# Kernel optimization log

Measured on AMD Instinct MI355X. Metric: run time of the kernel, lower is better.

## Reference

```python
import jax, jax.numpy as jnp
import numpy as np

N_HEADS = 12


def setup_inputs() -> dict:
    key = jax.random.key(0)
    ks = jax.random.split(key, 4)
    B, T, C = 1, 4096, 768
    x = jax.random.normal(ks[0], (B, T, C), dtype=jnp.float32)
    w_qkv = jax.random.normal(ks[1], (C, 3 * C), dtype=jnp.float32) * (C ** -0.5)
    b_qkv = jnp.zeros((3 * C,), dtype=jnp.float32)
    w_proj = jax.random.normal(ks[2], (C, C), dtype=jnp.float32) * (C ** -0.5)
    b_proj = jnp.zeros((C,), dtype=jnp.float32)
    return {"x": x, "w_qkv": w_qkv, "b_qkv": b_qkv, "w_proj": w_proj, "b_proj": b_proj}


def reference(x, w_qkv, b_qkv, w_proj, b_proj):
    B, T, C = x.shape
    H = N_HEADS
    hd = C // H
    qkv = x @ w_qkv + b_qkv                      # [B,T,3C]
    q, k, v = jnp.split(qkv, 3, axis=-1)
    # [B,H,T,hd]
    q = q.reshape(B, T, H, hd).transpose(0, 2, 1, 3)
    k = k.reshape(B, T, H, hd).transpose(0, 2, 1, 3)
    v = v.reshape(B, T, H, hd).transpose(0, 2, 1, 3)
    scale = 1.0 / jnp.sqrt(jnp.float32(hd))
    attn = jnp.einsum('bhqd,bhkd->bhqk', q, k) * scale  # [B,H,T,T]
    causal = jnp.tril(jnp.ones((T, T), dtype=bool))
    attn = jnp.where(causal, attn, jnp.float32(-jnp.inf))
    attn = jax.nn.softmax(attn, axis=-1)
    out = jnp.einsum('bhqk,bhkd->bhqd', attn, v)        # [B,H,T,hd]
    out = out.transpose(0, 2, 1, 3).reshape(B, T, C)
    return out @ w_proj + b_proj
```

## Files before the change

### kernel.cpp

```cpp
#include <hip/hip_runtime.h>
#include <hip/hip_bf16.h>


#define T_SEQ 4096
#define C_DIM 768
#define C3    2304
#define NH    12
#define HD    64

typedef __attribute__((ext_vector_type(8))) short bf16x8;
typedef __attribute__((ext_vector_type(4))) short bf16x4;
typedef __attribute__((ext_vector_type(4))) float f32x4;

__device__ inline unsigned short f2bf(float f) {
  union { float f; unsigned u; } v; v.f = f;
  unsigned r = v.u + 0x7fff + ((v.u >> 16) & 1);
  return (unsigned short)(r >> 16);
}
__device__ inline unsigned short f2bf_trunc(float f) {
  union { float f; unsigned u; } v; v.f = f;
  return (unsigned short)(v.u >> 16);
}

__device__ inline void gl2lds16(const void* g, void* l) {
  __builtin_amdgcn_global_load_lds(
      (const __attribute__((address_space(1))) unsigned int*)g,
      (__attribute__((address_space(3))) unsigned int*)l, 16, 0, 0);
}

#if __has_builtin(__builtin_amdgcn_exp2f)
#define EXP2F(x) __builtin_amdgcn_exp2f(x)
#else
#define EXP2F(x) exp2f(x)
#endif

#define NB_CONV  (T_SEQ * C_DIM / 2048)
#define NB_TQKV  ((C3 / 32) * (C_DIM / 32))
#define NB_TPROJ ((C_DIM / 32) * (C_DIM / 32))

__global__ __launch_bounds__(256) void prep_fused(
    const float* __restrict__ x, const float* __restrict__ w_qkv,
    const float* __restrict__ w_proj, unsigned short* __restrict__ xb,
    unsigned short* __restrict__ wqkvT, unsigned short* __restrict__ wprojT) {
  __shared__ float t[32][33];
  const int b = blockIdx.x;
  const int tid = threadIdx.x;

  if (b < NB_CONV) {
    int i = (b * 256 + tid) * 8;
    float4 v0 = *(const float4*)(x + i);
    float4 v1 = *(const float4*)(x + i + 4);
    unsigned short o[8] = {f2bf(v0.x), f2bf(v0.y), f2bf(v0.z), f2bf(v0.w),
                           f2bf(v1.x), f2bf(v1.y), f2bf(v1.z), f2bf(v1.w)};
    *(uint4*)(xb + i) = *(uint4*)o;
    return;
  }
  const float* in;
  unsigned short* outT;
  int R, Cc, bi;
  if (b < NB_CONV + NB_TQKV) {
    in = w_qkv; outT = wqkvT; R = C_DIM; Cc = C3; bi = b - NB_CONV;
  } else {
    in = w_proj; outT = wprojT; R = C_DIM; Cc = C_DIM; bi = b - NB_CONV - NB_TQKV;
  }
  const int tx = tid & 31, ty = tid >> 5;
  const int c0 = (bi % (Cc / 32)) * 32, r0 = (bi / (Cc / 32)) * 32;
#pragma unroll
  for (int i = 0; i < 4; ++i) {
    int r = ty + i * 8;
    t[r][tx] = in[(size_t)(r0 + r) * Cc + c0 + tx];
  }
  __syncthreads();
#pragma unroll
  for (int i = 0; i < 4; ++i) {
    int c = ty + i * 8;
    outT[(size_t)(c0 + c) * R + r0 + tx] = f2bf(t[tx][c]);
  }
}

__global__ __launch_bounds__(256) void gemm_qkv(
    const unsigned short* __restrict__ A, const unsigned short* __restrict__ Bt,
    const float* __restrict__ bias, unsigned short* __restrict__ Cq,
    unsigned short* __restrict__ vTp, int M, int N, int K) {
  __shared__ unsigned short As[128 * 64];
  __shared__ unsigned short Bs[128 * 64];
  const int tid = threadIdx.x;
  const int wave = tid >> 6, lane = tid & 63;
  const int lo = lane & 15, g8 = lane >> 4;
  const int lo7 = lo & 7;
  const int wm = wave >> 1, wn = wave & 1;
  const int bm = blockIdx.y * 128, bn = blockIdx.x * 128;
  const int drow8 = lane >> 3;
  const int dslot = (lane & 7) * 8;
  const int dsrc = ((lane & 7) ^ drow8) * 8;

  f32x4 acc[4][4];
#pragma unroll
  for (int mt = 0; mt < 4; ++mt)
#pragma unroll
    for (int nt = 0; nt < 4; ++nt) acc[mt][nt] = (f32x4){0.f, 0.f, 0.f, 0.f};

  const unsigned short* Abase = A + (size_t)bm * K;
  const unsigned short* Bbase = Bt + (size_t)bn * K;

  for (int k0 = 0; k0 < K; k0 += 64) {
    __syncthreads();
#pragma unroll
    for (int p = 0; p < 4; ++p) {
      const int r = p * 32 + wave * 8 + drow8;
      gl2lds16(Abase + (size_t)r * K + k0 + dsrc, As + r * 64 + dslot);
      gl2lds16(Bbase + (size_t)r * K + k0 + dsrc, Bs + r * 64 + dslot);
    }
    __syncthreads();

#pragma unroll
    for (int kk = 0; kk < 2; ++kk) {
      bf16x8 a[4], b[4];
#pragma unroll
      for (int mt = 0; mt < 4; ++mt)
        a[mt] = *(const bf16x8*)(
            As + (wm * 64 + mt * 16 + lo) * 64 + (((kk * 4 + g8) ^ lo7) * 8));
#pragma unroll
      for (int nt = 0; nt < 4; ++nt)
        b[nt] = *(const bf16x8*)(
            Bs + (wn * 64 + nt * 16 + lo) * 64 + (((kk * 4 + g8) ^ lo7) * 8));
#pragma unroll
      for (int mt = 0; mt < 4; ++mt)
#pragma unroll
        for (int nt = 0; nt < 4; ++nt)
          acc[mt][nt] = __builtin_amdgcn_mfma_f32_16x16x32_bf16(a[mt], b[nt], acc[mt][nt], 0, 0, 0);
    }
  }

  if (bn < 2 * C_DIM) {
    const float sc = (bn < C_DIM) ? 0.18033688011112042f : 1.0f;
#pragma unroll
    for (int nt = 0; nt < 4; ++nt) {
      const int n = bn + wn * 64 + nt * 16 + lo;
      const float bv = bias[n];
#pragma unroll
      for (int mt = 0; mt < 4; ++mt)
#pragma unroll
        for (int r = 0; r < 4; ++r) {
          const int m = bm + wm * 64 + mt * 16 + g8 * 4 + r;
          Cq[(size_t)m * C3 + n] = f2bf((acc[mt][nt][r] + bv) * sc);
        }
    }
  } else {
#pragma unroll
    for (int nt = 0; nt < 4; ++nt) {
      const int n = bn + wn * 64 + nt * 16 + lo;
      const float bv = bias[n];
      unsigned short* row = vTp + (size_t)(n - 2 * C_DIM) * T_SEQ;
#pragma unroll
      for (int mt = 0; mt < 4; ++mt) {
        const int mbase = (bm + wm * 64 + mt * 16 + g8 * 4) & ~31;
        bf16x4 o4;
#pragma unroll
        for (int r = 0; r < 4; ++r) o4[r] = (short)f2bf(acc[mt][nt][r] + bv);
        *(bf16x4*)(row + mbase + 8 * g8 + 4 * (mt & 1)) = o4;
      }
    }
  }
}

__global__ __launch_bounds__(256) void gemm_bt_mfma(
    const unsigned short* __restrict__ A, const unsigned short* __restrict__ Bt,
    const float* __restrict__ bias, float* __restrict__ C,
    int M, int N, int K) {
  __shared__ unsigned short As[128 * 64];
  __shared__ unsigned short Bs[128 * 64];
  const int tid = threadIdx.x;
  const int wave = tid >> 6, lane = tid & 63;
  const int lo = lane & 15, g8 = lane >> 4;
  const int lo7 = lo & 7;
  const int wm = wave >> 1, wn = wave & 1;
  const int bm = blockIdx.y * 128, bn = blockIdx.x * 128;
  const int drow8 = lane >> 3;
  const int dslot = (lane & 7) * 8;
  const int dsrc = ((lane & 7) ^ drow8) * 8;

  f32x4 acc[4][4];
#pragma unroll
  for (int mt = 0; mt < 4; ++mt)
#pragma unroll
    for (int nt = 0; nt < 4; ++nt) acc[mt][nt] = (f32x4){0.f, 0.f, 0.f, 0.f};

  const unsigned short* Abase = A + (size_t)bm * K;
  const unsigned short* Bbase = Bt + (size_t)bn * K;

  for (int k0 = 0; k0 < K; k0 += 64) {
    __syncthreads();
#pragma unroll
    for (int p = 0; p < 4; ++p) {
      const int r = p * 32 + wave * 8 + drow8;
      gl2lds16(Abase + (size_t)r * K + k0 + dsrc, As + r * 64 + dslot);
      gl2lds16(Bbase + (size_t)r * K + k0 + dsrc, Bs + r * 64 + dslot);
    }
    __syncthreads();

#pragma unroll
    for (int kk = 0; kk < 2; ++kk) {
      bf16x8 a[4], b[4];
#pragma unroll
      for (int mt = 0; mt < 4; ++mt)
        a[mt] = *(const bf16x8*)(
            As + (wm * 64 + mt * 16 + lo) * 64 + (((kk * 4 + g8) ^ lo7) * 8));
#pragma unroll
      for (int nt = 0; nt < 4; ++nt)
        b[nt] = *(const bf16x8*)(
            Bs + (wn * 64 + nt * 16 + lo) * 64 + (((kk * 4 + g8) ^ lo7) * 8));
#pragma unroll
      for (int mt = 0; mt < 4; ++mt)
#pragma unroll
        for (int nt = 0; nt < 4; ++nt)
          acc[mt][nt] = __builtin_amdgcn_mfma_f32_16x16x32_bf16(a[mt], b[nt], acc[mt][nt], 0, 0, 0);
    }
  }

#pragma unroll
  for (int nt = 0; nt < 4; ++nt) {
    const int n = bn + wn * 64 + nt * 16 + lo;
    const float bv = bias[n];
#pragma unroll
    for (int mt = 0; mt < 4; ++mt)
#pragma unroll
      for (int r = 0; r < 4; ++r) {
        const int m = bm + wm * 64 + mt * 16 + g8 * 4 + r;
        C[(size_t)m * N + n] = acc[mt][nt][r] + bv;
      }
  }
}

#define NREC   102
#define PO_REC (128 * 64)
#define KSTEP  (64 * C3)

__global__ __launch_bounds__(256) void flash_attn_d12(
    const unsigned short* __restrict__ qkv,
    const unsigned short* __restrict__ vTp,
    float* __restrict__ Po, float* __restrict__ Pl) {
  __shared__ unsigned short Ks[3][64 * 64];
  __shared__ unsigned short Vs[3][64 * 64];

  const int u = blockIdx.x;
  int h, qt, c;
  if (u < 900) {
    h = u / 75;
    const int w = u % 75;
    if (w < 15)      { qt = 29 + w / 5;          c = w % 5; }
    else if (w < 39) { const int r = w - 15; qt = 23 + r / 4; c = r % 4; }
    else if (w < 57) { const int r = w - 39; qt = 17 + r / 3; c = r % 3; }
    else if (w < 69) { const int r = w - 57; qt = 11 + r / 2; c = r % 2; }
    else             { qt = 5 + (w - 69);        c = 0; }
  } else {
    const int v = u - 900;
    int m, r;
    if (v < 60)       { m = 5; r = v; }
    else if (v < 120) { m = 4; r = v - 60; }
    else if (v < 180) { m = 3; r = v - 120; }
    else if (v < 252) { m = 2; r = v - 180; }
    else              { m = 1; r = v - 252; }
    const int per = (m >= 3) ? 5 : 6;
    h = r / per;
    qt = (m - 1) + 6 * (r % per);
    c = (qt + 1) / 6;
  }
  const int n = 2 * qt + 2;
  const int k0 = 12 * c;
  const int T = (n - k0 < 12) ? (n - k0) : 12;
  const int qt2 = 2 * qt;
  const int rec = c * (35 - 3 * c) + (qt - 6 * c);

  const int tid = threadIdx.x;
  const int w = tid >> 6;
  const int lane = tid & 63;
  const int lo = lane & 15;
  const int g = lane >> 4;
  const int lo7 = lo & 7;

  const unsigned short* Kg = qkv + C_DIM + h * HD;
  const unsigned short* Vg = vTp + (size_t)(h * HD) * T_SEQ;

  const int drow = tid >> 3;
  const int dslot = (tid & 7) * 8;
  const int dsrc = ((tid & 7) ^ (drow & 7)) * 8;

  const int qw0 = w * 32 + lo;
  bf16x8 qb[2][2];
#pragma unroll
  for (int qh = 0; qh < 2; ++qh)
#pragma unroll
    for (int dh = 0; dh < 2; ++dh)
      qb[qh][dh] = *(const bf16x8*)(
          qkv + (size_t)(qt * 128 + qw0 + qh * 16) * C3 + h * HD + dh * 32 + g * 8);

  const unsigned short* pK0 = Kg + (size_t)k0 * KSTEP + (size_t)drow * C3 + dsrc;
  const unsigned short* pK1 = pK0 + (size_t)32 * C3;
  const unsigned short* pV0 = Vg + (size_t)drow * T_SEQ + k0 * 64 + dsrc;
  const unsigned short* pV1 = pV0 + (size_t)32 * T_SEQ;

  auto stage = [&](int buf) __attribute__((always_inline)) {
    gl2lds16(pK0, Ks[buf] + drow * 64 + dslot);
    gl2lds16(pK1, Ks[buf] + (32 + drow) * 64 + dslot);
    gl2lds16(pV0, Vs[buf] + drow * 64 + dslot);
    gl2lds16(pV1, Vs[buf] + (32 + drow) * 64 + dslot);
    pK0 += KSTEP; pK1 += KSTEP; pV0 += 64; pV1 += 64;
  };

  bf16x8 onesb;
#pragma unroll
  for (int e = 0; e < 8; ++e) onesb[e] = (short)0x3F80;

  stage(0);
  stage(1);
  asm volatile("s_waitcnt vmcnt(4)" ::: "memory");
  __builtin_amdgcn_s_barrier();

  f32x4 o_acc[2][4];
  f32x4 lacc[2];
#pragma unroll
  for (int qh = 0; qh < 2; ++qh) {
    lacc[qh] = (f32x4){0.f, 0.f, 0.f, 0.f};
#pragma unroll
    for (int dt = 0; dt < 4; ++dt) o_acc[qh][dt] = (f32x4){0.f, 0.f, 0.f, 0.f};
  }

  int ic = 0, iw = 2;
  int ktc = k0;
  for (int t = 0; t < T; ++t) {
    if (t + 2 < T) stage(iw);
    const unsigned short* Kc = Ks[ic];
    const unsigned short* Vc = Vs[ic];

    f32x4 st[2][4];
#pragma unroll
    for (int qh = 0; qh < 2; ++qh)
#pragma unroll
      for (int mt = 0; mt < 4; ++mt) st[qh][mt] = (f32x4){0.f, 0.f, 0.f, 0.f};
    __builtin_amdgcn_s_setprio(1);
#pragma unroll
    for (int mt = 0; mt < 4; ++mt)
#pragma unroll
      for (int dh = 0; dh < 2; ++dh) {
        bf16x8 a = *(const bf16x8*)(
            Kc + (mt * 16 + lo) * 64 + (((dh * 4 + g) ^ lo7) * 8));
#pragma unroll
        for (int qh = 0; qh < 2; ++qh)
          st[qh][mt] = __builtin_amdgcn_mfma_f32_16x16x32_bf16(
              a, qb[qh][dh], st[qh][mt], 0, 0, 0);
      }
    __builtin_amdgcn_s_setprio(0);

    if (ktc >= qt2) {
      const int mb = (ktc == qt2) ? 0 : 64;
#pragma unroll
      for (int qh = 0; qh < 2; ++qh) {
        const int qr = qw0 + qh * 16;
#pragma unroll
        for (int mt = 0; mt < 4; ++mt)
#pragma unroll
          for (int r = 0; r < 4; ++r)
            if (mb + mt * 16 + g * 4 + r > qr) st[qh][mt][r] = -1e30f;
      }
    }

    bf16x8 pt[2][2];
#pragma unroll
    for (int qh = 0; qh < 2; ++qh)
#pragma unroll
      for (int kh = 0; kh < 2; ++kh)
#pragma unroll
        for (int jj = 0; jj < 4; ++jj) {
          float e0 = EXP2F(st[qh][kh * 2][jj]);
          float e1 = EXP2F(st[qh][kh * 2 + 1][jj]);
          pt[qh][kh][jj] = (short)f2bf_trunc(e0);
          pt[qh][kh][4 + jj] = (short)f2bf_trunc(e1);
        }

    __builtin_amdgcn_s_setprio(1);
#pragma unroll
    for (int qh = 0; qh < 2; ++qh) {
      lacc[qh] = __builtin_amdgcn_mfma_f32_16x16x32_bf16(onesb, pt[qh][0], lacc[qh], 0, 0, 0);
      lacc[qh] = __builtin_amdgcn_mfma_f32_16x16x32_bf16(onesb, pt[qh][1], lacc[qh], 0, 0, 0);
    }
#pragma unroll
    for (int dt = 0; dt < 4; ++dt)
#pragma unroll
      for (int kh = 0; kh < 2; ++kh) {
        bf16x8 av = *(const bf16x8*)(
            Vc + (dt * 16 + lo) * 64 + (((kh * 4 + g) ^ lo7) * 8));
#pragma unroll
        for (int qh = 0; qh < 2; ++qh)
          o_acc[qh][dt] = __builtin_amdgcn_mfma_f32_16x16x32_bf16(
              av, pt[qh][kh], o_acc[qh][dt], 0, 0, 0);
      }
    __builtin_amdgcn_s_setprio(0);

    if (t + 2 < T)
      asm volatile("s_waitcnt vmcnt(4)" ::: "memory");
    else
      asm volatile("s_waitcnt vmcnt(0)" ::: "memory");
    __builtin_amdgcn_s_barrier();

    ic = (ic == 2) ? 0 : ic + 1;
    iw = (iw == 2) ? 0 : iw + 1;
    ++ktc;
  }

  float* PoS = Po + ((size_t)h * NREC + rec) * PO_REC;
#pragma unroll
  for (int qh = 0; qh < 2; ++qh)
#pragma unroll
    for (int dt = 0; dt < 4; ++dt)
      *(f32x4*)(PoS + (qw0 + qh * 16) * 64 + dt * 16 + g * 4) = o_acc[qh][dt];
  if (g == 0) {
    float* PlS = Pl + ((size_t)h * NREC + rec) * 128;
#pragma unroll
    for (int qh = 0; qh < 2; ++qh) PlS[qw0 + qh * 16] = lacc[qh][0];
  }
}

__global__ __launch_bounds__(256) void combine_d12(
    const float* __restrict__ Po, const float* __restrict__ Pl,
    unsigned short* __restrict__ out) {
  const int bid = blockIdx.x;
  const int h = bid >> 5, qt = bid & 31;
  const int tid = threadIdx.x;
  const int q = tid >> 1;
  const int c0 = (tid & 1) * 32;
  const int cmax = qt / 6;
  float l = 0.f;
  f32x4 acc[8];
#pragma unroll
  for (int e = 0; e < 8; ++e) acc[e] = (f32x4){0.f, 0.f, 0.f, 0.f};
  for (int c = 0; c <= cmax; ++c) {
    const int rec = c * (35 - 3 * c) + (qt - 6 * c);
    const size_t base = (size_t)h * NREC + rec;
    l += Pl[base * 128 + q];
    const float* P = Po + base * PO_REC + q * 64 + c0;
#pragma unroll
    for (int e = 0; e < 8; ++e) acc[e] += *(const f32x4*)(P + e * 4);
  }
  const float inv = 1.0f / l;
  unsigned short ob[32];
#pragma unroll
  for (int e = 0; e < 8; ++e)
#pragma unroll
    for (int r = 0; r < 4; ++r) ob[e * 4 + r] = f2bf(acc[e][r] * inv);
  unsigned short* op = out + (size_t)(qt * 128 + q) * C_DIM + h * 64 + c0;
#pragma unroll
  for (int e2 = 0; e2 < 4; ++e2)
    *(uint4*)(op + e2 * 8) = *(uint4*)(ob + e2 * 8);
}

extern "C" void kernel_launch(void* const* d_in, const int* in_sizes, int n_in,
                              void* d_out, int out_size, void* d_ws, size_t ws_size,
                              hipStream_t stream) {
  const float* x      = (const float*)d_in[0];
  const float* w_qkv  = (const float*)d_in[1];
  const float* b_qkv  = (const float*)d_in[2];
  const float* w_proj = (const float*)d_in[3];
  const float* b_proj = (const float*)d_in[4];
  float* out = (float*)d_out;

  unsigned short* xb     = (unsigned short*)d_ws;
  unsigned short* wqkvT  = xb + (size_t)T_SEQ * C_DIM;
  unsigned short* wprojT = wqkvT + (size_t)C3 * C_DIM;
  unsigned short* qkv    = wprojT + (size_t)C_DIM * C_DIM;
  unsigned short* vTp    = qkv + (size_t)T_SEQ * C3;
  unsigned short* attnb  = xb;
  float* Po = (float*)(vTp + (size_t)C_DIM * T_SEQ);
  float* Pl = Po + (size_t)NH * NREC * PO_REC;

  prep_fused<<<NB_CONV + NB_TQKV + NB_TPROJ, 256, 0, stream>>>(
      x, w_qkv, w_proj, xb, wqkvT, wprojT);

  gemm_qkv<<<dim3(C3 / 128, T_SEQ / 128), 256, 0, stream>>>(
      xb, wqkvT, b_qkv, qkv, vTp, T_SEQ, C3, C_DIM);

  flash_attn_d12<<<1224, 256, 0, stream>>>(qkv, vTp, Po, Pl);

  combine_d12<<<NH * 32, 256, 0, stream>>>(Po, Pl, attnb);

  gemm_bt_mfma<<<dim3(C_DIM / 128, T_SEQ / 128), 256, 0, stream>>>(
      attnb, wprojT, b_proj, out, T_SEQ, C_DIM, C_DIM);
}
```

Before: 187.1 us.

## Double attention query tile to 256 rows with 512-thread blocks

Reworks the split-KV flash attention so each block processes 256 query rows using 8 waves of 512 threads instead of 128 rows, with a new work decomposition into 612 blocks and matching partial-record layout. Each K/V tile staged in LDS is now reused by twice as many query rows, halving global K/V traffic per query and halving the number of partial records the combine kernel must reduce. The causal mask is generalized to several diagonal tiles. In exchange it has fewer, larger blocks with more masked diagonal work and possibly worse load balance and occupancy.

```diff
diff --git a/kernel.cpp b/kernel.cpp
--- a/kernel.cpp
+++ b/kernel.cpp
@@ -232,11 +232,16 @@
   }
 }
 
-#define NREC   102
-#define PO_REC (128 * 64)
+#define NRECH  51
+#define PO_REC (256 * 64)
 #define KSTEP  (64 * C3)
 
-__global__ __launch_bounds__(256) void flash_attn_d12(
+__device__ inline int s_pref(int qt) {
+  const int A = qt / 3, B = qt - 3 * A;
+  return qt + 3 * A * (A - 1) / 2 + A * B;
+}
+
+__global__ __launch_bounds__(512, 6) void flash_attn_qb256(
     const unsigned short* __restrict__ qkv,
     const unsigned short* __restrict__ vTp,
     float* __restrict__ Po, float* __restrict__ Pl) {
@@ -244,33 +249,26 @@
   __shared__ unsigned short Vs[3][64 * 64];
 
   const int u = blockIdx.x;
-  int h, qt, c;
-  if (u < 900) {
-    h = u / 75;
-    const int w = u % 75;
-    if (w < 15)      { qt = 29 + w / 5;          c = w % 5; }
-    else if (w < 39) { const int r = w - 15; qt = 23 + r / 4; c = r % 4; }
-    else if (w < 57) { const int r = w - 39; qt = 17 + r / 3; c = r % 3; }
-    else if (w < 69) { const int r = w - 57; qt = 11 + r / 2; c = r % 2; }
-    else             { qt = 5 + (w - 69);        c = 0; }
+  int h, qt, c, k0, T;
+  if (u < 480) {
+    h = u / 40;
+    const int w40 = u % 40;
+    qt = 2; c = 0;
+    for (int q = 15; q >= 2; --q) {
+      const int A = q / 3, B = q - 3 * A;
+      const int F = 3 * A * (A - 1) / 2 + A * (B + 1);
+      if (w40 >= F) { qt = q; c = w40 - F; break; }
+    }
+    k0 = 12 * c; T = 12;
+  } else if (u < 540) {
+    const int v = u - 480; h = v / 5; const int e = v % 5;
+    qt = 3 * e + 1; c = e; k0 = 12 * e; T = 8;
   } else {
-    const int v = u - 900;
-    int m, r;
-    if (v < 60)       { m = 5; r = v; }
-    else if (v < 120) { m = 4; r = v - 60; }
-    else if (v < 180) { m = 3; r = v - 120; }
-    else if (v < 252) { m = 2; r = v - 180; }
-    else              { m = 1; r = v - 252; }
-    const int per = (m >= 3) ? 5 : 6;
-    h = r / per;
-    qt = (m - 1) + 6 * (r % per);
-    c = (qt + 1) / 6;
-  }
-  const int n = 2 * qt + 2;
-  const int k0 = 12 * c;
-  const int T = (n - k0 < 12) ? (n - k0) : 12;
-  const int qt2 = 2 * qt;
-  const int rec = c * (35 - 3 * c) + (qt - 6 * c);
+    const int v = u - 540; h = v / 6; const int e = v % 6;
+    qt = 3 * e; c = e; k0 = 12 * e; T = 4;
+  }
+  const int rec = h * NRECH + s_pref(qt) + c;
+  const int qt4 = 4 * qt;
 
   const int tid = threadIdx.x;
   const int w = tid >> 6;
@@ -293,19 +291,15 @@
 #pragma unroll
     for (int dh = 0; dh < 2; ++dh)
       qb[qh][dh] = *(const bf16x8*)(
-          qkv + (size_t)(qt * 128 + qw0 + qh * 16) * C3 + h * HD + dh * 32 + g * 8);
-
-  const unsigned short* pK0 = Kg + (size_t)k0 * KSTEP + (size_t)drow * C3 + dsrc;
-  const unsigned short* pK1 = pK0 + (size_t)32 * C3;
-  const unsigned short* pV0 = Vg + (size_t)drow * T_SEQ + k0 * 64 + dsrc;
-  const unsigned short* pV1 = pV0 + (size_t)32 * T_SEQ;
+          qkv + (size_t)(qt * 256 + qw0 + qh * 16) * C3 + h * HD + dh * 32 + g * 8);
+
+  const unsigned short* pK = Kg + (size_t)(k0 * 64 + drow) * C3 + dsrc;
+  const unsigned short* pV = Vg + (size_t)drow * T_SEQ + k0 * 64 + dsrc;
 
   auto stage = [&](int buf) __attribute__((always_inline)) {
-    gl2lds16(pK0, Ks[buf] + drow * 64 + dslot);
-    gl2lds16(pK1, Ks[buf] + (32 + drow) * 64 + dslot);
-    gl2lds16(pV0, Vs[buf] + drow * 64 + dslot);
-    gl2lds16(pV1, Vs[buf] + (32 + drow) * 64 + dslot);
-    pK0 += KSTEP; pK1 += KSTEP; pV0 += 64; pV1 += 64;
+    gl2lds16(pK, Ks[buf] + drow * 64 + dslot);
+    gl2lds16(pV, Vs[buf] + drow * 64 + dslot);
+    pK += KSTEP; pV += 64;
   };
 
   bf16x8 onesb;
@@ -314,7 +308,7 @@
 
   stage(0);
   stage(1);
-  asm volatile("s_waitcnt vmcnt(4)" ::: "memory");
+  asm volatile("s_waitcnt vmcnt(2)" ::: "memory");
   __builtin_amdgcn_s_barrier();
 
   f32x4 o_acc[2][4];
@@ -352,8 +346,8 @@
       }
     __builtin_amdgcn_s_setprio(0);
 
-    if (ktc >= qt2) {
-      const int mb = (ktc == qt2) ? 0 : 64;
+    if (ktc >= qt4) {
+      const int mb = (ktc - qt4) * 64;
 #pragma unroll
       for (int qh = 0; qh < 2; ++qh) {
         const int qr = qw0 + qh * 16;
@@ -398,7 +392,7 @@
     __builtin_amdgcn_s_setprio(0);
 
     if (t + 2 < T)
-      asm volatile("s_waitcnt vmcnt(4)" ::: "memory");
+      asm volatile("s_waitcnt vmcnt(2)" ::: "memory");
     else
       asm volatile("s_waitcnt vmcnt(0)" ::: "memory");
     __builtin_amdgcn_s_barrier();
@@ -408,50 +402,53 @@
     ++ktc;
   }
 
-  float* PoS = Po + ((size_t)h * NREC + rec) * PO_REC;
+  float* PoS = Po + (size_t)rec * PO_REC;
 #pragma unroll
   for (int qh = 0; qh < 2; ++qh)
 #pragma unroll
     for (int dt = 0; dt < 4; ++dt)
       *(f32x4*)(PoS + (qw0 + qh * 16) * 64 + dt * 16 + g * 4) = o_acc[qh][dt];
   if (g == 0) {
-    float* PlS = Pl + ((size_t)h * NREC + rec) * 128;
+    float* PlS = Pl + (size_t)rec * 256;
 #pragma unroll
     for (int qh = 0; qh < 2; ++qh) PlS[qw0 + qh * 16] = lacc[qh][0];
   }
 }
 
-__global__ __launch_bounds__(256) void combine_d12(
+__global__ __launch_bounds__(256) void combine_qb256(
     const float* __restrict__ Po, const float* __restrict__ Pl,
     unsigned short* __restrict__ out) {
   const int bid = blockIdx.x;
-  const int h = bid >> 5, qt = bid & 31;
+  const int h = bid >> 4, qt = bid & 15;
+  const int nc = qt / 3 + 1;
+  const int rec0 = h * NRECH + s_pref(qt);
   const int tid = threadIdx.x;
-  const int q = tid >> 1;
-  const int c0 = (tid & 1) * 32;
-  const int cmax = qt / 6;
-  float l = 0.f;
-  f32x4 acc[8];
-#pragma unroll
-  for (int e = 0; e < 8; ++e) acc[e] = (f32x4){0.f, 0.f, 0.f, 0.f};
-  for (int c = 0; c <= cmax; ++c) {
-    const int rec = c * (35 - 3 * c) + (qt - 6 * c);
-    const size_t base = (size_t)h * NREC + rec;
-    l += Pl[base * 128 + q];
-    const float* P = Po + base * PO_REC + q * 64 + c0;
-#pragma unroll
-    for (int e = 0; e < 8; ++e) acc[e] += *(const f32x4*)(P + e * 4);
-  }
-  const float inv = 1.0f / l;
-  unsigned short ob[32];
-#pragma unroll
-  for (int e = 0; e < 8; ++e)
-#pragma unroll
-    for (int r = 0; r < 4; ++r) ob[e * 4 + r] = f2bf(acc[e][r] * inv);
-  unsigned short* op = out + (size_t)(qt * 128 + q) * C_DIM + h * 64 + c0;
-#pragma unroll
-  for (int e2 = 0; e2 < 4; ++e2)
-    *(uint4*)(op + e2 * 8) = *(uint4*)(ob + e2 * 8);
+  const int q0 = tid >> 2;
+  const int c0 = (tid & 3) * 16;
+#pragma unroll
+  for (int qq = 0; qq < 4; ++qq) {
+    const int q = qq * 64 + q0;
+    float l = 0.f;
+    f32x4 acc[4];
+#pragma unroll
+    for (int e = 0; e < 4; ++e) acc[e] = (f32x4){0.f, 0.f, 0.f, 0.f};
+    for (int c = 0; c < nc; ++c) {
+      const size_t base = (size_t)(rec0 + c);
+      l += Pl[base * 256 + q];
+      const float* P = Po + base * PO_REC + q * 64 + c0;
+#pragma unroll
+      for (int e = 0; e < 4; ++e) acc[e] += *(const f32x4*)(P + e * 4);
+    }
+    const float inv = 1.0f / l;
+    unsigned short ob[16];
+#pragma unroll
+    for (int e = 0; e < 4; ++e)
+#pragma unroll
+      for (int r = 0; r < 4; ++r) ob[e * 4 + r] = f2bf(acc[e][r] * inv);
+    unsigned short* op = out + (size_t)(qt * 256 + q) * C_DIM + h * 64 + c0;
+    *(uint4*)op = *(uint4*)ob;
+    *(uint4*)(op + 8) = *(uint4*)(ob + 8);
+  }
 }
 
 extern "C" void kernel_launch(void* const* d_in, const int* in_sizes, int n_in,
@@ -471,7 +468,7 @@
   unsigned short* vTp    = qkv + (size_t)T_SEQ * C3;
   unsigned short* attnb  = xb;
   float* Po = (float*)(vTp + (size_t)C_DIM * T_SEQ);
-  float* Pl = Po + (size_t)NH * NREC * PO_REC;
+  float* Pl = Po + (size_t)NH * NRECH * PO_REC;
 
   prep_fused<<<NB_CONV + NB_TQKV + NB_TPROJ, 256, 0, stream>>>(
       x, w_qkv, w_proj, xb, wqkvT, wprojT);
@@ -479,9 +476,9 @@
   gemm_qkv<<<dim3(C3 / 128, T_SEQ / 128), 256, 0, stream>>>(
       xb, wqkvT, b_qkv, qkv, vTp, T_SEQ, C3, C_DIM);
 
-  flash_attn_d12<<<1224, 256, 0, stream>>>(qkv, vTp, Po, Pl);
-
-  combine_d12<<<NH * 32, 256, 0, stream>>>(Po, Pl, attnb);
+  flash_attn_qb256<<<612, 512, 0, stream>>>(qkv, vTp, Po, Pl);
+
+  combine_qb256<<<NH * 16, 256, 0, stream>>>(Po, Pl, attnb);
 
   gemm_bt_mfma<<<dim3(C_DIM / 128, T_SEQ / 128), 256, 0, stream>>>(
       attnb, wprojT, b_proj, out, T_SEQ, C_DIM, C_DIM);
```

Measured after the change: 301.0 us. 1.61x slower.
